# Optimization experiments

Measured on AMD Instinct MI355X. Metric: run time of the kernel, lower is better.

Reference implementation:

```python
import jax, jax.numpy as jnp
import numpy as np

ALPHA = 0.2  # leaky_relu negative slope
NEG = -1e20


def gat_conv(x, edges, W, a, b):
    # x: [B,N,F], W: [F,O], a: [2O,1], b: [O]
    h = jnp.einsum('bnf,fo->bno', x, W)
    O = W.shape[1]
    # cat([h[src], h[tgt]]) @ a  ==  h[src]@a[:O] + h[tgt]@a[O:]
    s1 = h @ a[:O, 0]   # [B,N]
    s2 = h @ a[O:, 0]   # [B,N]
    src, tgt = edges[0], edges[1]
    e = jax.nn.leaky_relu(s1[:, src] + s2[:, tgt], ALPHA)  # [B,E]
    B, N, _ = h.shape
    # dense NxN scatter-assign, as in the original module
    att = jnp.full((B, N, N), NEG, dtype=h.dtype).at[:, src, tgt].set(e)
    att = jax.nn.softmax(att, axis=-1)
    return jnp.einsum('bnm,bmo->bno', att, h) + b


def setup_inputs() -> dict:
    key = jax.random.key(0)
    ks = jax.random.split(key, 8)
    B, N, E = 2, 2048, 32768
    Fin, nhid, nhead, Fout = 256, 8, 8, 64
    x = jax.random.normal(ks[0], (B, N, Fin), dtype=jnp.float32)
    edges = jax.random.randint(ks[1], (2, E), 0, N)
    # xavier-like init (gain 1.414)
    W_h = jax.random.normal(ks[2], (nhead, Fin, nhid), dtype=jnp.float32) * (1.414 / np.sqrt(Fin))
    a_h = jax.random.normal(ks[3], (nhead, 2 * nhid, 1), dtype=jnp.float32) * 0.3
    b_h = jnp.zeros((nhead, nhid), dtype=jnp.float32)
    W_o = jax.random.normal(ks[4], (nhid * nhead, Fout), dtype=jnp.float32) * (1.414 / np.sqrt(nhid * nhead))
    a_o = jax.random.normal(ks[5], (2 * Fout, 1), dtype=jnp.float32) * 0.1
    b_o = jnp.zeros((Fout,), dtype=jnp.float32)
    return {'x': x, 'edges': edges, 'W_h': W_h, 'a_h': a_h, 'b_h': b_h,
            'W_o': W_o, 'a_o': a_o, 'b_o': b_o}


def reference(x, edges, W_h, a_h, b_h, W_o, a_o, b_o):
    B, N, _ = x.shape
    # nhead parallel GATConv heads, concatenated along feature dim
    heads = jax.vmap(lambda W, a, b: gat_conv(x, edges, W, a, b))(W_h, a_h, b_h)  # [H,B,N,nhid]
    x1 = jax.nn.elu(jnp.moveaxis(heads, 0, 2).reshape(B, N, -1))  # [B,N,H*nhid]
    out = gat_conv(x1, edges, W_o, a_o, b_o)  # single out head (mean of 1)
    return jax.nn.log_softmax(out, axis=1)  # softmax over the node dim, per original
```

## Files before the change

kernel.cpp:

```cpp
#include <hip/hip_runtime.h>

#define BB   2
#define NN   2048
#define FIN  256
#define HH   8
#define NHID 8
#define C1   64
#define FOUT 64
#define MAXD 192

__global__ __launch_bounds__(256)
void k_front(const float* __restrict__ x, const float* __restrict__ Wh,
             const float* __restrict__ ah, const int* __restrict__ edges, int E,
             float* __restrict__ h1, float* __restrict__ s1h, float* __restrict__ s2h,
             int* __restrict__ cnt, int* __restrict__ csr)
{
    __shared__ float xs[16][FIN];
    int tid = threadIdx.x;

    if (blockIdx.x >= 256) {
        int e = (blockIdx.x - 256) * 256 + tid;
        if (e < E) {
            int s = edges[e], t = edges[E + e];
            int pos = atomicAdd(&cnt[s], 1);
            if (pos < MAXD) csr[s * MAXD + pos] = t;
        }
        return;
    }

    int base = blockIdx.x * 16;
    const float4* xv = (const float4*)(x + (size_t)base * FIN);
    float4* xsv = (float4*)&xs[0][0];
#pragma unroll
    for (int i = 0; i < 4; ++i) xsv[tid + 256 * i] = xv[tid + 256 * i];
    __syncthreads();

    int wave = tid >> 6, lane = tid & 63;
    int head = lane >> 3, k = lane & 7;
    const float* Wp = Wh + head * FIN * NHID + k;
    int n0 = wave * 4;
    float a0 = 0.f, a1 = 0.f, a2 = 0.f, a3 = 0.f;
#pragma unroll 4
    for (int f = 0; f < FIN; ++f) {
        float wv = Wp[f * NHID];
        a0 += wv * xs[n0 + 0][f];
        a1 += wv * xs[n0 + 1][f];
        a2 += wv * xs[n0 + 2][f];
        a3 += wv * xs[n0 + 3][f];
    }
    size_t hb = (size_t)(base + n0) * C1 + lane;
    h1[hb] = a0; h1[hb + C1] = a1; h1[hb + 2 * C1] = a2; h1[hb + 3 * C1] = a3;

    float c1 = ah[head * 16 + k], c2 = ah[head * 16 + 8 + k];
    float p0 = a0 * c1, p1 = a1 * c1, p2 = a2 * c1, p3 = a3 * c1;
    float q0 = a0 * c2, q1 = a1 * c2, q2 = a2 * c2, q3 = a3 * c2;
    for (int o = 1; o < 8; o <<= 1) {
        p0 += __shfl_xor(p0, o); p1 += __shfl_xor(p1, o);
        p2 += __shfl_xor(p2, o); p3 += __shfl_xor(p3, o);
        q0 += __shfl_xor(q0, o); q1 += __shfl_xor(q1, o);
        q2 += __shfl_xor(q2, o); q3 += __shfl_xor(q3, o);
    }
    if (k == 0) {
        float ps[4] = {p0, p1, p2, p3}, qs[4] = {q0, q1, q2, q3};
#pragma unroll
        for (int j = 0; j < 4; ++j) {
            int bn = base + n0 + j;
            int b = bn >> 11, n = bn & (NN - 1);
            s1h[(b * HH + head) * NN + n] = ps[j];
            s2h[(b * HH + head) * NN + n] = qs[j];
        }
    }
}

__global__ __launch_bounds__(256)
void k_att1g2(const float* __restrict__ h1, const float* __restrict__ s1h,
              const float* __restrict__ s2h, const float* __restrict__ bh,
              const int* __restrict__ cnt, const int* __restrict__ csr,
              const float* __restrict__ Wo, const float* __restrict__ ao,
              float* __restrict__ h2, float* __restrict__ s1o, float* __restrict__ s2o)
{
    __shared__ int tg4[4][MAXD];
    __shared__ float xs4[4][C1];
    int tid = threadIdx.x, w = tid >> 6, lane = tid & 63;
    int* tg = tg4[w];
    float* xs = xs4[w];
    int bn = blockIdx.x * 4 + w;
    int b = bn >> 11, n = bn & (NN - 1);
    int head = lane >> 3;

    int d = cnt[n]; if (d > MAXD) d = MAXD;
    for (int l = lane; l < d; l += 64) tg[l] = csr[n * MAXD + l];
    for (int l = lane; l < d; l += 64) {
        int t = tg[l], f = 0;
        for (int j = 0; j < l; ++j) f |= (tg[j] == t);
        if (f) tg[l] = -1;
    }

    const float* hp = h1 + (size_t)b * NN * C1 + lane;
    float out;
    if (d == 0) {
        float acc = 0.f;
        for (int j = 0; j < NN; ++j) acc += hp[(size_t)j * C1];
        out = acc * (1.0f / NN);
    } else {
        float s1 = s1h[(b * HH + head) * NN + n];
        const float* s2p = s2h + (b * HH + head) * NN;
        float m = -3.4e38f;
        for (int p = 0; p < d; ++p) {
            int t = tg[p]; if (t < 0) continue;
            float ee = s1 + s2p[t];
            ee = ee > 0.f ? ee : 0.2f * ee;
            m = fmaxf(m, ee);
        }
        float den = 0.f, acc = 0.f;
        for (int p = 0; p < d; ++p) {
            int t = tg[p]; if (t < 0) continue;
            float ee = s1 + s2p[t];
            ee = ee > 0.f ? ee : 0.2f * ee;
            float wt = expf(ee - m);
            den += wt;
            acc += wt * hp[(size_t)t * C1];
        }
        out = acc / den;
    }
    out += bh[lane];
    xs[lane] = out > 0.f ? out : (expf(out) - 1.f);

    float acc2 = 0.f;
#pragma unroll 16
    for (int f = 0; f < C1; ++f) acc2 += xs[f] * Wo[f * FOUT + lane];
    h2[(size_t)bn * FOUT + lane] = acc2;
    float p = acc2 * ao[lane];
    float q = acc2 * ao[FOUT + lane];
    for (int o = 1; o < 64; o <<= 1) { p += __shfl_xor(p, o); q += __shfl_xor(q, o); }
    if (lane == 0) { s1o[bn] = p; s2o[bn] = q; }
}

__global__ __launch_bounds__(256)
void k_att2(const float* __restrict__ h2, const float* __restrict__ s1o,
            const float* __restrict__ s2o, const float* __restrict__ bo,
            const int* __restrict__ cnt, const int* __restrict__ csr,
            float* __restrict__ out2T)
{
    __shared__ int tg4[4][MAXD];
    int tid = threadIdx.x, w = tid >> 6, lane = tid & 63;
    int* tg = tg4[w];
    int bn = blockIdx.x * 4 + w;
    int b = bn >> 11, n = bn & (NN - 1);

    int d = cnt[n]; if (d > MAXD) d = MAXD;
    for (int l = lane; l < d; l += 64) tg[l] = csr[n * MAXD + l];
    for (int l = lane; l < d; l += 64) {
        int t = tg[l], f = 0;
        for (int j = 0; j < l; ++j) f |= (tg[j] == t);
        if (f) tg[l] = -1;
    }

    const float* hp = h2 + (size_t)b * NN * FOUT + lane;
    float out;
    if (d == 0) {
        float acc = 0.f;
        for (int j = 0; j < NN; ++j) acc += hp[(size_t)j * FOUT];
        out = acc * (1.0f / NN);
    } else {
        float s1 = s1o[bn];
        const float* s2p = s2o + b * NN;
        float m = -3.4e38f;
        for (int p = 0; p < d; ++p) {
            int t = tg[p]; if (t < 0) continue;
            float ee = s1 + s2p[t];
            ee = ee > 0.f ? ee : 0.2f * ee;
            m = fmaxf(m, ee);
        }
        float den = 0.f, acc = 0.f;
        for (int p = 0; p < d; ++p) {
            int t = tg[p]; if (t < 0) continue;
            float ee = s1 + s2p[t];
            ee = ee > 0.f ? ee : 0.2f * ee;
            float wt = expf(ee - m);
            den += wt;
            acc += wt * hp[(size_t)t * FOUT];
        }
        out = acc / den;
    }
    out2T[(size_t)(b * FOUT + lane) * NN + n] = out + bo[lane];
}

__global__ __launch_bounds__(256)
void k_lsef(const float* __restrict__ out2T, float* __restrict__ out)
{
    int row = blockIdx.x;
    int b = row >> 6, o = row & 63;
    int tid = threadIdx.x;
    const float* p = out2T + (size_t)row * NN;
    float v[8];
    float m = -3.4e38f;
#pragma unroll
    for (int j = 0; j < 8; ++j) {
        v[j] = p[tid + 256 * j];
        m = fmaxf(m, v[j]);
    }
    for (int off = 1; off < 64; off <<= 1) m = fmaxf(m, __shfl_xor(m, off));
    __shared__ float sm[4], ss[4];
    if ((tid & 63) == 0) sm[tid >> 6] = m;
    __syncthreads();
    float M = fmaxf(fmaxf(sm[0], sm[1]), fmaxf(sm[2], sm[3]));
    float sum = 0.f;
#pragma unroll
    for (int j = 0; j < 8; ++j) sum += expf(v[j] - M);
    for (int off = 1; off < 64; off <<= 1) sum += __shfl_xor(sum, off);
    if ((tid & 63) == 0) ss[tid >> 6] = sum;
    __syncthreads();
    float lse = M + logf(ss[0] + ss[1] + ss[2] + ss[3]);
    float* op = out + (size_t)b * NN * FOUT + o;
#pragma unroll
    for (int j = 0; j < 8; ++j) op[(size_t)(tid + 256 * j) * FOUT] = v[j] - lse;
}

extern "C" void kernel_launch(void* const* d_in, const int* in_sizes, int n_in,
                              void* d_out, int out_size, void* d_ws, size_t ws_size,
                              hipStream_t stream)
{
    (void)n_in; (void)out_size; (void)ws_size;
    const float* x     = (const float*)d_in[0];
    const int*   edges = (const int*)d_in[1];
    const float* Wh    = (const float*)d_in[2];
    const float* ah    = (const float*)d_in[3];
    const float* bh    = (const float*)d_in[4];
    const float* Wo    = (const float*)d_in[5];
    const float* ao    = (const float*)d_in[6];
    const float* bo    = (const float*)d_in[7];
    int E = in_sizes[1] / 2;

    char* w = (char*)d_ws;
    float* h1    = (float*)w; w += (size_t)BB * NN * C1 * 4;
    float* s1h   = (float*)w; w += (size_t)BB * HH * NN * 4;
    float* s2h   = (float*)w; w += (size_t)BB * HH * NN * 4;
    float* h2    = (float*)w; w += (size_t)BB * NN * FOUT * 4;
    float* s1o   = (float*)w; w += (size_t)BB * NN * 4;
    float* s2o   = (float*)w; w += (size_t)BB * NN * 4;
    float* out2T = (float*)w; w += (size_t)BB * FOUT * NN * 4;
    int*   cnt   = (int*)w;   w += (size_t)NN * 4;
    int*   csr   = (int*)w;   w += (size_t)NN * MAXD * 4;

    hipMemsetAsync(cnt, 0, (size_t)NN * 4, stream);

    int scatter_blocks = (E + 255) / 256;
    k_front <<<256 + scatter_blocks, 256, 0, stream>>>(x, Wh, ah, edges, E,
                                                       h1, s1h, s2h, cnt, csr);
    k_att1g2<<<BB * NN / 4, 256, 0, stream>>>(h1, s1h, s2h, bh, cnt, csr,
                                              Wo, ao, h2, s1o, s2o);
    k_att2  <<<BB * NN / 4, 256, 0, stream>>>(h2, s1o, s2o, bo, cnt, csr, out2T);
    k_lsef  <<<BB * FOUT, 256, 0, stream>>>(out2T, (float*)d_out);
}
```

Before: 136.6 us.

## Vectorize front GEMV, reuse dedup edge lists, add fast gather path

```diff
diff --git a/kernel.cpp b/kernel.cpp
--- a/kernel.cpp
+++ b/kernel.cpp
@@ -8,6 +8,7 @@
 #define C1   64
 #define FOUT 64
 #define MAXD 192
+#define FASTD 64
 
 __global__ __launch_bounds__(256)
 void k_front(const float* __restrict__ x, const float* __restrict__ Wh,
@@ -39,14 +40,22 @@
     int head = lane >> 3, k = lane & 7;
     const float* Wp = Wh + head * FIN * NHID + k;
     int n0 = wave * 4;
+    const float4* xr0 = (const float4*)xs[n0 + 0];
+    const float4* xr1 = (const float4*)xs[n0 + 1];
+    const float4* xr2 = (const float4*)xs[n0 + 2];
+    const float4* xr3 = (const float4*)xs[n0 + 3];
     float a0 = 0.f, a1 = 0.f, a2 = 0.f, a3 = 0.f;
-#pragma unroll 4
-    for (int f = 0; f < FIN; ++f) {
-        float wv = Wp[f * NHID];
-        a0 += wv * xs[n0 + 0][f];
-        a1 += wv * xs[n0 + 1][f];
-        a2 += wv * xs[n0 + 2][f];
-        a3 += wv * xs[n0 + 3][f];
+#pragma unroll 8
+    for (int ff = 0; ff < FIN / 4; ++ff) {
+        float4 v0 = xr0[ff], v1 = xr1[ff], v2 = xr2[ff], v3 = xr3[ff];
+        float w0 = Wp[(4 * ff + 0) * NHID];
+        float w1 = Wp[(4 * ff + 1) * NHID];
+        float w2 = Wp[(4 * ff + 2) * NHID];
+        float w3 = Wp[(4 * ff + 3) * NHID];
+        a0 += w0 * v0.x; a0 += w1 * v0.y; a0 += w2 * v0.z; a0 += w3 * v0.w;
+        a1 += w0 * v1.x; a1 += w1 * v1.y; a1 += w2 * v1.z; a1 += w3 * v1.w;
+        a2 += w0 * v2.x; a2 += w1 * v2.y; a2 += w2 * v2.z; a2 += w3 * v2.w;
+        a3 += w0 * v3.x; a3 += w1 * v3.y; a3 += w2 * v3.z; a3 += w3 * v3.w;
     }
     size_t hb = (size_t)(base + n0) * C1 + lane;
     h1[hb] = a0; h1[hb + C1] = a1; h1[hb + 2 * C1] = a2; h1[hb + 3 * C1] = a3;
@@ -75,11 +84,12 @@
 __global__ __launch_bounds__(256)
 void k_att1g2(const float* __restrict__ h1, const float* __restrict__ s1h,
               const float* __restrict__ s2h, const float* __restrict__ bh,
-              const int* __restrict__ cnt, const int* __restrict__ csr,
+              const int* __restrict__ cnt, int* __restrict__ csr,
               const float* __restrict__ Wo, const float* __restrict__ ao,
               float* __restrict__ h2, float* __restrict__ s1o, float* __restrict__ s2o)
 {
     __shared__ int tg4[4][MAXD];
+    __shared__ float es4[4][FASTD][HH];
     __shared__ float xs4[4][C1];
     int tid = threadIdx.x, w = tid >> 6, lane = tid & 63;
     int* tg = tg4[w];
@@ -95,6 +105,7 @@
         for (int j = 0; j < l; ++j) f |= (tg[j] == t);
         if (f) tg[l] = -1;
     }
+    for (int l = lane; l < d; l += 64) csr[n * MAXD + l] = tg[l];
 
     const float* hp = h1 + (size_t)b * NN * C1 + lane;
     float out;
@@ -102,6 +113,50 @@
         float acc = 0.f;
         for (int j = 0; j < NN; ++j) acc += hp[(size_t)j * C1];
         out = acc * (1.0f / NN);
+    } else if (d <= FASTD) {
+        const float* s2b = s2h + (size_t)b * HH * NN;
+        for (int idx = lane; idx < d * HH; idx += 64) {
+            int l = idx >> 3, hh = idx & 7;
+            int t = tg[l];
+            es4[w][l][hh] = s2b[hh * NN + (t < 0 ? 0 : t)];
+        }
+        float s1 = s1h[(b * HH + head) * NN + n];
+        float m = -3.4e38f;
+        for (int p = 0; p < d; ++p) {
+            float ee = s1 + es4[w][p][head];
+            ee = ee > 0.f ? ee : 0.2f * ee;
+            m = fmaxf(m, tg[p] < 0 ? -3.4e38f : ee);
+        }
+        float den = 0.f, acc = 0.f;
+        int p = 0;
+        for (; p + 4 <= d; p += 4) {
+            int t0 = tg[p], t1 = tg[p + 1], t2 = tg[p + 2], t3 = tg[p + 3];
+            float v0 = hp[(size_t)(t0 < 0 ? 0 : t0) * C1];
+            float v1 = hp[(size_t)(t1 < 0 ? 0 : t1) * C1];
+            float v2 = hp[(size_t)(t2 < 0 ? 0 : t2) * C1];
+            float v3 = hp[(size_t)(t3 < 0 ? 0 : t3) * C1];
+            float e0 = s1 + es4[w][p + 0][head]; e0 = e0 > 0.f ? e0 : 0.2f * e0;
+            float e1 = s1 + es4[w][p + 1][head]; e1 = e1 > 0.f ? e1 : 0.2f * e1;
+            float e2 = s1 + es4[w][p + 2][head]; e2 = e2 > 0.f ? e2 : 0.2f * e2;
+            float e3 = s1 + es4[w][p + 3][head]; e3 = e3 > 0.f ? e3 : 0.2f * e3;
+            float w0 = t0 < 0 ? 0.f : expf(e0 - m);
+            float w1 = t1 < 0 ? 0.f : expf(e1 - m);
+            float w2 = t2 < 0 ? 0.f : expf(e2 - m);
+            float w3 = t3 < 0 ? 0.f : expf(e3 - m);
+            den += w0; acc += w0 * v0;
+            den += w1; acc += w1 * v1;
+            den += w2; acc += w2 * v2;
+            den += w3; acc += w3 * v3;
+        }
+        for (; p < d; ++p) {
+            int t = tg[p];
+            float v = hp[(size_t)(t < 0 ? 0 : t) * C1];
+            float ee = s1 + es4[w][p][head];
+            ee = ee > 0.f ? ee : 0.2f * ee;
+            float wt = t < 0 ? 0.f : expf(ee - m);
+            den += wt; acc += wt * v;
+        }
+        out = acc / den;
     } else {
         float s1 = s1h[(b * HH + head) * NN + n];
         const float* s2p = s2h + (b * HH + head) * NN;
@@ -143,6 +198,7 @@
             float* __restrict__ out2T)
 {
     __shared__ int tg4[4][MAXD];
+    __shared__ float es4[4][FASTD];
     int tid = threadIdx.x, w = tid >> 6, lane = tid & 63;
     int* tg = tg4[w];
     int bn = blockIdx.x * 4 + w;
@@ -150,21 +206,58 @@
 
     int d = cnt[n]; if (d > MAXD) d = MAXD;
     for (int l = lane; l < d; l += 64) tg[l] = csr[n * MAXD + l];
-    for (int l = lane; l < d; l += 64) {
-        int t = tg[l], f = 0;
-        for (int j = 0; j < l; ++j) f |= (tg[j] == t);
-        if (f) tg[l] = -1;
-    }
 
     const float* hp = h2 + (size_t)b * NN * FOUT + lane;
+    const float* s2p = s2o + b * NN;
     float out;
     if (d == 0) {
         float acc = 0.f;
         for (int j = 0; j < NN; ++j) acc += hp[(size_t)j * FOUT];
         out = acc * (1.0f / NN);
+    } else if (d <= FASTD) {
+        for (int l = lane; l < d; l += 64) {
+            int t = tg[l];
+            es4[w][l] = s2p[t < 0 ? 0 : t];
+        }
+        float s1 = s1o[bn];
+        float m = -3.4e38f;
+        for (int p = 0; p < d; ++p) {
+            float ee = s1 + es4[w][p];
+            ee = ee > 0.f ? ee : 0.2f * ee;
+            m = fmaxf(m, tg[p] < 0 ? -3.4e38f : ee);
+        }
+        float den = 0.f, acc = 0.f;
+        int p = 0;
+        for (; p + 4 <= d; p += 4) {
+            int t0 = tg[p], t1 = tg[p + 1], t2 = tg[p + 2], t3 = tg[p + 3];
+            float v0 = hp[(size_t)(t0 < 0 ? 0 : t0) * FOUT];
+            float v1 = hp[(size_t)(t1 < 0 ? 0 : t1) * FOUT];
+            float v2 = hp[(size_t)(t2 < 0 ? 0 : t2) * FOUT];
+            float v3 = hp[(size_t)(t3 < 0 ? 0 : t3) * FOUT];
+            float e0 = s1 + es4[w][p + 0]; e0 = e0 > 0.f ? e0 : 0.2f * e0;
+            float e1 = s1 + es4[w][p + 1]; e1 = e1 > 0.f ? e1 : 0.2f * e1;
+            float e2 = s1 + es4[w][p + 2]; e2 = e2 > 0.f ? e2 : 0.2f * e2;
+            float e3 = s1 + es4[w][p + 3]; e3 = e3 > 0.f ? e3 : 0.2f * e3;
+            float w0 = t0 < 0 ? 0.f : expf(e0 - m);
+            float w1 = t1 < 0 ? 0.f : expf(e1 - m);
+            float w2 = t2 < 0 ? 0.f : expf(e2 - m);
+            float w3 = t3 < 0 ? 0.f : expf(e3 - m);
+            den += w0; acc += w0 * v0;
+            den += w1; acc += w1 * v1;
+            den += w2; acc += w2 * v2;
+            den += w3; acc += w3 * v3;
+        }
+        for (; p < d; ++p) {
+            int t = tg[p];
+            float v = hp[(size_t)(t < 0 ? 0 : t) * FOUT];
+            float ee = s1 + es4[w][p];
+            ee = ee > 0.f ? ee : 0.2f * ee;
+            float wt = t < 0 ? 0.f : expf(ee - m);
+            den += wt; acc += wt * v;
+        }
+        out = acc / den;
     } else {
         float s1 = s1o[bn];
-        const float* s2p = s2o + b * NN;
         float m = -3.4e38f;
         for (int p = 0; p < d; ++p) {
             int t = tg[p]; if (t < 0) continue;
```

Result: faster. 113.7 us (-16.8%).
